# Performance work log

Hardware: AMD Instinct MI355X
Metric: run time of the kernel (lower is better)

## Reference

```python
import jax, jax.numpy as jnp
import numpy as np

H = W = 28
PI = np.pi


def _encoder(x, c1w, c1b, c2w, c2b):
    dn = ('NCHW', 'OIHW', 'NCHW')
    h = jax.lax.conv_general_dilated(x, c1w, (1, 1), 'SAME', dimension_numbers=dn)
    h = jax.nn.relu(h + c1b[None, :, None, None])
    h = jax.lax.conv_general_dilated(h, c2w, (2, 2), 'SAME', dimension_numbers=dn)
    return jax.nn.relu(h + c2b[None, :, None, None])


def _angles_deg(x):
    # Batched replacement of the per-image masked-point PCA loop:
    # masked 2x2 covariance + closed-form top eigenvector (same math as
    # torch.svd of the mean-centered selected points).
    B = x.shape[0]
    imgs = x.reshape(B, -1)                       # [B, 784]
    m = (imgs > 0.5).astype(x.dtype)              # boolean selection as weights
    xs = jnp.linspace(-14.0, 14.0, 28)
    ys = jnp.linspace(14.0, -14.0, 28)
    gx, gy = jnp.meshgrid(xs, ys)                 # 'xy' indexing, matches np.meshgrid
    gx = gx.reshape(-1)
    gy = gy.reshape(-1)                           # [784]
    n = jnp.maximum(m.sum(1), 1.0)                # [B]
    mx = (m * gx).sum(1) / n
    my = (m * gy).sum(1) / n
    dx = gx[None, :] - mx[:, None]                # [B, 784]
    dy = gy[None, :] - my[:, None]
    a = (m * dx * dx).sum(1)                      # unnormalized covariance entries
    b = (m * dx * dy).sum(1)
    c = (m * dy * dy).sum(1)
    lam = 0.5 * (a + c) + jnp.sqrt(0.25 * (a - c) ** 2 + b * b)  # top eigenvalue
    v1 = jnp.stack([b, lam - a], -1)              # two algebraic eigenvector forms
    v2 = jnp.stack([lam - c, b], -1)
    use1 = (v1 * v1).sum(-1) >= (v2 * v2).sum(-1)
    v = jnp.where(use1[:, None], v1, v2)
    v = jnp.where((v * v).sum(-1, keepdims=True) < 1e-12,
                  jnp.array([1.0, 0.0], dtype=x.dtype), v)  # isotropic fallback
    return jnp.arctan2(v[:, 1], v[:, 0]) * (180.0 / PI)


def _rotate(x, angles_deg):
    # kornia.geometry.rotate: rotate by angle degrees (CCW) about image center,
    # bilinear interpolation, zero padding. x: [B,1,H,W].
    B = x.shape[0]
    th = angles_deg * (PI / 180.0)
    cs = jnp.cos(th)[:, None, None]
    sn = jnp.sin(th)[:, None, None]
    yy, xx = jnp.meshgrid(jnp.arange(H, dtype=x.dtype),
                          jnp.arange(W, dtype=x.dtype), indexing='ij')
    cx = (W - 1) / 2.0
    cy = (H - 1) / 2.0
    dxp = xx - cx
    dyp = yy - cy
    # inverse warp (OpenCV getRotationMatrix2D convention)
    sx = cs * dxp + sn * dyp + cx                 # [B,H,W] source coords
    sy = -sn * dxp + cs * dyp + cy
    x0 = jnp.floor(sx)
    y0 = jnp.floor(sy)
    wx1 = sx - x0
    wx0 = 1.0 - wx1
    wy1 = sy - y0
    wy0 = 1.0 - wy1
    img = x.reshape(B, -1)                        # single channel

    def samp(yi, xi):
        valid = (xi >= 0) & (xi <= W - 1) & (yi >= 0) & (yi <= H - 1)
        xi_ = jnp.clip(xi, 0, W - 1).astype(jnp.int32)
        yi_ = jnp.clip(yi, 0, H - 1).astype(jnp.int32)
        idx = (yi_ * W + xi_).reshape(B, -1)
        vals = jnp.take_along_axis(img, idx, axis=1).reshape(B, H, W)
        return vals * valid.astype(x.dtype)

    out = (samp(y0, x0) * wy0 * wx0 + samp(y0, x0 + 1) * wy0 * wx1 +
           samp(y0 + 1, x0) * wy1 * wx0 + samp(y0 + 1, x0 + 1) * wy1 * wx1)
    return out[:, None, :, :]


def setup_inputs() -> dict:
    key = jax.random.key(0)
    ks = jax.random.split(key, 5)
    B = 2048
    x = jax.random.uniform(ks[0], (B, 1, 28, 28), jnp.float32)
    conv1_w = jax.random.normal(ks[1], (32, 1, 3, 3), jnp.float32) * 0.1
    conv1_b = jnp.zeros((32,), jnp.float32)
    conv2_w = jax.random.normal(ks[2], (64, 32, 3, 3), jnp.float32) * 0.05
    conv2_b = jnp.zeros((64,), jnp.float32)
    pred_w = jax.random.normal(ks[3], (64 * 14 * 14, 10), jnp.float32) * 0.01
    pred_b = jnp.zeros((10,), jnp.float32)
    return {'x': x, 'conv1_w': conv1_w, 'conv1_b': conv1_b,
            'conv2_w': conv2_w, 'conv2_b': conv2_b,
            'pred_w': pred_w, 'pred_b': pred_b}


def reference(x, conv1_w, conv1_b, conv2_w, conv2_b, pred_w, pred_b):
    angles = jax.lax.stop_gradient(_angles_deg(x))  # original detaches angles
    x_canonized = _rotate(x, -angles)
    reps = _encoder(x_canonized, conv1_w, conv1_b, conv2_w, conv2_b)
    reps = reps.reshape(x.shape[0], -1)             # [B, 12544]
    return reps @ pred_w + pred_b                   # [B, 10]
```

## Files before the change

### kernel.cpp

```cpp
#include <hip/hip_runtime.h>
#include <math.h>

typedef __attribute__((ext_vector_type(8))) short short8;
typedef __attribute__((ext_vector_type(4))) float f32x4;
typedef __attribute__((ext_vector_type(8))) _Float16 half8;
typedef __attribute__((ext_vector_type(4))) _Float16 half4;
typedef __attribute__((ext_vector_type(2))) _Float16 half2v;
typedef __attribute__((ext_vector_type(4))) unsigned int uint4v;

#define H1_OFF   3840
#define H1_ROWB  1920
#define LDS_BYTES (H1_OFF + 29*H1_ROWB)
#define RED_OFF  25344

__device__ __forceinline__ int h1_byte(int y, int x, int chunk) {
    int b = H1_OFF + y*H1_ROWB + x*64 + chunk*16;
    return b ^ (((x >> 1) & 7) << 4);
}

__device__ __forceinline__ half2v hmax2(half2v a) {
#if defined(__has_builtin) && __has_builtin(__builtin_elementwise_max)
    half2v z = {(_Float16)0.0f, (_Float16)0.0f};
    return __builtin_elementwise_max(a, z);
#else
    half2v r;
    r[0] = a[0] > (_Float16)0.0f ? a[0] : (_Float16)0.0f;
    r[1] = a[1] > (_Float16)0.0f ? a[1] : (_Float16)0.0f;
    return r;
#endif
}

__global__ __launch_bounds__(256) void prep_kernel(
    const float* __restrict__ w1, const float* __restrict__ b1,
    const float* __restrict__ w2, const float* __restrict__ pw,
    unsigned* __restrict__ w1pk,
    unsigned short* __restrict__ w2frag, unsigned short* __restrict__ pwt2)
{
    const int NW1 = 160;
    const int NW2 = 9*4*64*8;
    const int NPW = 10*12544;
    for (int idx = blockIdx.x*256 + threadIdx.x; idx < NW1 + NW2 + NPW; idx += gridDim.x*256) {
        if (idx < NW1) {
            half2v h;
            if (idx < 144) {
                int c2 = idx / 9, k = idx - 9*c2;
                h[0] = (_Float16)w1[(2*c2)*9 + k];
                h[1] = (_Float16)w1[(2*c2+1)*9 + k];
            } else {
                int c2 = idx - 144;
                h[0] = (_Float16)b1[2*c2];
                h[1] = (_Float16)b1[2*c2+1];
            }
            w1pk[idx] = __builtin_bit_cast(unsigned, h);
        } else if (idx < NW1 + NW2) {
            int d = idx - NW1;
            int m = d & 7;
            int l = (d >> 3) & 63;
            int f = d >> 9;
            int oct = f & 3;
            int kk = f >> 2;
            int oc = oct*16 + (l & 15);
            int c  = (l >> 4)*8 + m;
            _Float16 h = (_Float16)w2[(oc*32 + c)*9 + kk];
            w2frag[d] = __builtin_bit_cast(unsigned short, h);
        } else {
            int j = idx - NW1 - NW2;
            int k = j / 12544;
            int i2 = j - k*12544;
            _Float16 h = (_Float16)pw[i2*10 + k];
            pwt2[k*12544 + i2] = __builtin_bit_cast(unsigned short, h);
        }
    }
}

__global__ __launch_bounds__(256) void angle_kernel(
    const float* __restrict__ x, float2* __restrict__ csn)
{
    const int b = blockIdx.x;
    const int t = threadIdx.x;
    const float* xb = x + b * 784;

    double S = 0, Sx = 0, Sy = 0, Sxx = 0, Sxy = 0, Syy = 0;
    for (int p = t; p < 784; p += 256) {
        float v = xb[p];
        if (v > 0.5f) {
            int j = p / 28;
            int i = p - j * 28;
            double gx = -14.0 + i * (28.0 / 27.0);
            double gy =  14.0 - j * (28.0 / 27.0);
            S   += 1.0;
            Sx  += gx;   Sy  += gy;
            Sxx += gx * gx; Sxy += gx * gy; Syy += gy * gy;
        }
    }
    #pragma unroll
    for (int off = 32; off; off >>= 1) {
        S   += __shfl_down(S, off);
        Sx  += __shfl_down(Sx, off);
        Sy  += __shfl_down(Sy, off);
        Sxx += __shfl_down(Sxx, off);
        Sxy += __shfl_down(Sxy, off);
        Syy += __shfl_down(Syy, off);
    }
    __shared__ double red[4][6];
    const int lane = t & 63, w = t >> 6;
    if (lane == 0) {
        red[w][0] = S; red[w][1] = Sx; red[w][2] = Sy;
        red[w][3] = Sxx; red[w][4] = Sxy; red[w][5] = Syy;
    }
    __syncthreads();
    if (t == 0) {
        S   = red[0][0] + red[1][0] + red[2][0] + red[3][0];
        Sx  = red[0][1] + red[1][1] + red[2][1] + red[3][1];
        Sy  = red[0][2] + red[1][2] + red[2][2] + red[3][2];
        Sxx = red[0][3] + red[1][3] + red[2][3] + red[3][3];
        Sxy = red[0][4] + red[1][4] + red[2][4] + red[3][4];
        Syy = red[0][5] + red[1][5] + red[2][5] + red[3][5];

        double n  = (S < 1.0) ? 1.0 : S;
        double mx = Sx / n, my = Sy / n;
        double a  = Sxx - 2.0 * mx * Sx + mx * mx * S;
        double bb = Sxy - mx * Sy - my * Sx + mx * my * S;
        double cc = Syy - 2.0 * my * Sy + my * my * S;
        double lam = 0.5 * (a + cc) + sqrt(0.25 * (a - cc) * (a - cc) + bb * bb);
        double v1x = bb, v1y = lam - a;
        double v2x = lam - cc, v2y = bb;
        double n1 = v1x * v1x + v1y * v1y;
        double n2 = v2x * v2x + v2y * v2y;
        double vx, vy;
        if (n1 >= n2) { vx = v1x; vy = v1y; } else { vx = v2x; vy = v2y; }
        if (vx * vx + vy * vy < 1e-12) { vx = 1.0; vy = 0.0; }
        double th = -atan2(vy, vx);
        csn[b] = make_float2((float)cos(th), (float)sin(th));
    }
}

__global__ __launch_bounds__(1024, 8) void fused_kernel(
    const float* __restrict__ x,
    const unsigned* __restrict__ w1pk,
    const float* __restrict__ b2,
    const unsigned short* __restrict__ w2frag,
    const unsigned short* __restrict__ pwt2,
    const float* __restrict__ pb,
    const float2* __restrict__ csn,
    float* __restrict__ out)
{
    __shared__ __align__(16) char lds[LDS_BYTES];
    float* rotf = (float*)lds;
    float* imgf = (float*)(lds + H1_OFF);
    _Float16* reps16 = (_Float16*)lds;
    float* red  = (float*)(lds + RED_OFF);

    const int b = blockIdx.x;
    const int t = threadIdx.x;
    const int lane = t & 63;
    const int wv = t >> 6;
    const int l15 = lane & 15;
    const int g   = lane >> 4;

    const float* xb = x + b*784;
    int ty = t/28, tx = t - ty*28;
    if (t < 784) {
        imgf[ty*32 + tx] = xb[t];
    }
    if (t < 960) rotf[t] = 0.0f;
    __syncthreads();

    if (t < 784) {
        const float2 cn = csn[b];
        const float cs = cn.x, sn = cn.y;
        float dxp = (float)tx - 13.5f;
        float dyp = (float)ty - 13.5f;
        float sx =  cs*dxp + sn*dyp + 13.5f;
        float sy = -sn*dxp + cs*dyp + 13.5f;
        float x0 = floorf(sx), y0 = floorf(sy);
        float wx1 = sx - x0, wx0 = 1.0f - wx1;
        float wy1 = sy - y0, wy0 = 1.0f - wy1;
        int ix0 = (int)x0, iy0 = (int)y0;
        int ix1 = ix0 + 1, iy1 = iy0 + 1;
        int cx0 = min(max(ix0, 0), 27), cy0 = min(max(iy0, 0), 27);
        int cx1 = min(max(ix1, 0), 27), cy1 = min(max(iy1, 0), 27);
        bool vx0 = (ix0 >= 0) & (ix0 <= 27);
        bool vx1 = (ix1 >= 0) & (ix1 <= 27);
        bool vy0 = (iy0 >= 0) & (iy0 <= 27);
        bool vy1 = (iy1 >= 0) & (iy1 <= 27);
        float a00 = imgf[cy0*32 + cx0];
        float a01 = imgf[cy0*32 + cx1];
        float a10 = imgf[cy1*32 + cx0];
        float a11 = imgf[cy1*32 + cx1];
        float v00 = (vx0 & vy0) ? a00 : 0.f;
        float v01 = (vx1 & vy0) ? a01 : 0.f;
        float v10 = (vx0 & vy1) ? a10 : 0.f;
        float v11 = (vx1 & vy1) ? a11 : 0.f;
        float r = v00*wy0*wx0 + v01*wy0*wx1 + v10*wy1*wx0 + v11*wy1*wx1;
        rotf[(ty + 1)*32 + (tx + 1)] = r;
    }
    __syncthreads();

    if (t < 228) {
        short8 z8 = {0,0,0,0,0,0,0,0};
        int cell = t >> 2;
        int chunk = t & 3;
        int y, xx;
        if (cell < 29) { y = 28; xx = cell; } else { y = cell - 29; xx = 28; }
        *(short8*)(lds + h1_byte(y, xx, chunk)) = z8;
    }

    if (lane < 49) {
        int p = wv*49 + lane;
        int py = p/28, px = p - py*28;
        const float* rp = rotf + py*32 + px;
        half2v rs[9];
        {
            float rv[9] = { rp[0],  rp[1],  rp[2],
                            rp[32], rp[33], rp[34],
                            rp[64], rp[65], rp[66] };
            #pragma unroll
            for (int m = 0; m < 9; ++m) {
                _Float16 h = (_Float16)rv[m];
                rs[m][0] = h; rs[m][1] = h;
            }
        }
        half2v acc2[16];
        #pragma unroll
        for (int c2 = 0; c2 < 16; ++c2) {
            half2v a = __builtin_bit_cast(half2v, w1pk[144 + c2]);
            #pragma unroll
            for (int k = 0; k < 9; ++k) {
                half2v w = __builtin_bit_cast(half2v, w1pk[c2*9 + k]);
                a = w * rs[k] + a;
            }
            acc2[c2] = hmax2(a);
        }
        #pragma unroll
        for (int c8 = 0; c8 < 4; ++c8) {
            uint4v vh;
            #pragma unroll
            for (int j = 0; j < 4; ++j)
                vh[j] = __builtin_bit_cast(unsigned, acc2[c8*4 + j]);
            *(uint4v*)(lds + h1_byte(py, px, c8)) = vh;
        }
    }
    __syncthreads();

    const int oct = wv & 3;
    const int trow = wv >> 2;
    const int nq = (trow == 0) ? 4 : 3;
    int oyq[4], oxq[4];
    #pragma unroll
    for (int q = 0; q < 4; ++q) {
        int sp = (trow + 4*q)*16 + l15;
        sp = sp > 195 ? 195 : sp;
        oyq[q] = sp/14;
        oxq[q] = sp - 14*oyq[q];
    }
    f32x4 acc[4];
    #pragma unroll
    for (int q = 0; q < 4; ++q) acc[q] = (f32x4){0.f, 0.f, 0.f, 0.f};

    for (int kk = 0; kk < 9; ++kk) {
        int ky = kk/3;
        int kx = kk - ky*3;
        half8 bh = *(const half8*)(w2frag + (kk*4 + oct)*512 + lane*8);
        #pragma unroll
        for (int q = 0; q < 4; ++q) {
            if (q < nq) {
                int y = 2*oyq[q] + ky, xx = 2*oxq[q] + kx;
                half8 ah = *(const half8*)(lds + h1_byte(y, xx, g));
                acc[q] = __builtin_amdgcn_mfma_f32_16x16x32_f16(ah, bh, acc[q], 0, 0, 0);
            }
        }
    }
    __syncthreads();

    {
        int oc = oct*16 + l15;
        float bias = b2[oc];
        #pragma unroll
        for (int q = 0; q < 4; ++q) {
            if (q < nq) {
                int sp0 = (trow + 4*q)*16 + 4*g;
                if (sp0 + 3 < 196) {
                    half4 v;
                    #pragma unroll
                    for (int j = 0; j < 4; ++j)
                        v[j] = (_Float16)fmaxf(acc[q][j] + bias, 0.0f);
                    *(half4*)(reps16 + oc*196 + sp0) = v;
                }
            }
        }
    }
    __syncthreads();

    float a10[10];
    #pragma unroll
    for (int k = 0; k < 10; ++k) a10[k] = 0.0f;
    const unsigned* pw32 = (const unsigned*)pwt2;
    const unsigned* rp32 = (const unsigned*)reps16;
    for (int ip = t; ip < 6272; ip += 1024) {
        unsigned rv = rp32[ip];
#if defined(__has_builtin) && __has_builtin(__builtin_amdgcn_fdot2)
        half2v rh = __builtin_bit_cast(half2v, rv);
        #pragma unroll
        for (int k = 0; k < 10; ++k) {
            half2v ph = __builtin_bit_cast(half2v, pw32[k*6272 + ip]);
            a10[k] = __builtin_amdgcn_fdot2(rh, ph, a10[k], false);
        }
#else
        half2v rh = __builtin_bit_cast(half2v, rv);
        float r0 = (float)rh[0], r1 = (float)rh[1];
        #pragma unroll
        for (int k = 0; k < 10; ++k) {
            half2v ph = __builtin_bit_cast(half2v, pw32[k*6272 + ip]);
            a10[k] = fmaf(r0, (float)ph[0], fmaf(r1, (float)ph[1], a10[k]));
        }
#endif
    }
    #pragma unroll
    for (int k = 0; k < 10; ++k) {
        float v = a10[k];
        #pragma unroll
        for (int off = 32; off; off >>= 1) v += __shfl_down(v, off);
        a10[k] = v;
    }
    if (lane == 0) {
        #pragma unroll
        for (int k = 0; k < 10; ++k) red[wv*10 + k] = a10[k];
    }
    __syncthreads();
    if (t < 10) {
        float s = pb[t];
        #pragma unroll
        for (int w = 0; w < 16; ++w) s += red[w*10 + t];
        out[b*10 + t] = s;
    }
}

extern "C" void kernel_launch(void* const* d_in, const int* in_sizes, int n_in,
                              void* d_out, int out_size, void* d_ws, size_t ws_size,
                              hipStream_t stream)
{
    const float* x   = (const float*)d_in[0];
    const float* w1  = (const float*)d_in[1];
    const float* b1  = (const float*)d_in[2];
    const float* w2  = (const float*)d_in[3];
    const float* b2  = (const float*)d_in[4];
    const float* pw  = (const float*)d_in[5];
    const float* pb  = (const float*)d_in[6];
    float* out = (float*)d_out;

    const int B = in_sizes[0] / 784;

    char* wsb = (char*)d_ws;
    float2* csn = (float2*)wsb;
    unsigned* w1pk = (unsigned*)(wsb + (size_t)B*8);
    unsigned short* w2frag = (unsigned short*)(wsb + (size_t)B*8 + 640);
    unsigned short* pwt2   = (unsigned short*)(wsb + (size_t)B*8 + 640 + 36864);

    prep_kernel<<<563, 256, 0, stream>>>(w1, b1, w2, pw, w1pk, w2frag, pwt2);
    angle_kernel<<<B, 256, 0, stream>>>(x, csn);
    fused_kernel<<<B, 1024, 0, stream>>>(x, w1pk, b2, w2frag, pwt2, pb, csn, out);
}
```

Baseline: 81.79 us.

## Fuse angle PCA reduction into main kernel and drop separate angle launch

Moves the per-image masked covariance reduction and eigenvector computation into the fused kernel, using the already-loaded image pixels, wave shuffles and an LDS cross-wave reduce. This removes one kernel launch, the second read of x, and the csn round-trip through global memory. It also replaces atan2/cos/sin with direct normalisation of the eigenvector. The cost is an extra barrier and a serial double-precision tail inside the main kernel, with LDS slots reused for the reduction.

```diff
diff --git a/kernel.cpp b/kernel.cpp
--- a/kernel.cpp
+++ b/kernel.cpp
@@ -11,6 +11,8 @@
 #define H1_OFF   3840
 #define H1_ROWB  1920
 #define LDS_BYTES (H1_OFF + 29*H1_ROWB)
+#define ANG_OFF  7424
+#define CSN_OFF  8192
 #define RED_OFF  25344
 
 __device__ __forceinline__ int h1_byte(int y, int x, int chunk) {
@@ -73,68 +75,6 @@
     }
 }
 
-__global__ __launch_bounds__(256) void angle_kernel(
-    const float* __restrict__ x, float2* __restrict__ csn)
-{
-    const int b = blockIdx.x;
-    const int t = threadIdx.x;
-    const float* xb = x + b * 784;
-
-    double S = 0, Sx = 0, Sy = 0, Sxx = 0, Sxy = 0, Syy = 0;
-    for (int p = t; p < 784; p += 256) {
-        float v = xb[p];
-        if (v > 0.5f) {
-            int j = p / 28;
-            int i = p - j * 28;
-            double gx = -14.0 + i * (28.0 / 27.0);
-            double gy =  14.0 - j * (28.0 / 27.0);
-            S   += 1.0;
-            Sx  += gx;   Sy  += gy;
-            Sxx += gx * gx; Sxy += gx * gy; Syy += gy * gy;
-        }
-    }
-    #pragma unroll
-    for (int off = 32; off; off >>= 1) {
-        S   += __shfl_down(S, off);
-        Sx  += __shfl_down(Sx, off);
-        Sy  += __shfl_down(Sy, off);
-        Sxx += __shfl_down(Sxx, off);
-        Sxy += __shfl_down(Sxy, off);
-        Syy += __shfl_down(Syy, off);
-    }
-    __shared__ double red[4][6];
-    const int lane = t & 63, w = t >> 6;
-    if (lane == 0) {
-        red[w][0] = S; red[w][1] = Sx; red[w][2] = Sy;
-        red[w][3] = Sxx; red[w][4] = Sxy; red[w][5] = Syy;
-    }
-    __syncthreads();
-    if (t == 0) {
-        S   = red[0][0] + red[1][0] + red[2][0] + red[3][0];
-        Sx  = red[0][1] + red[1][1] + red[2][1] + red[3][1];
-        Sy  = red[0][2] + red[1][2] + red[2][2] + red[3][2];
-        Sxx = red[0][3] + red[1][3] + red[2][3] + red[3][3];
-        Sxy = red[0][4] + red[1][4] + red[2][4] + red[3][4];
-        Syy = red[0][5] + red[1][5] + red[2][5] + red[3][5];
-
-        double n  = (S < 1.0) ? 1.0 : S;
-        double mx = Sx / n, my = Sy / n;
-        double a  = Sxx - 2.0 * mx * Sx + mx * mx * S;
-        double bb = Sxy - mx * Sy - my * Sx + mx * my * S;
-        double cc = Syy - 2.0 * my * Sy + my * my * S;
-        double lam = 0.5 * (a + cc) + sqrt(0.25 * (a - cc) * (a - cc) + bb * bb);
-        double v1x = bb, v1y = lam - a;
-        double v2x = lam - cc, v2y = bb;
-        double n1 = v1x * v1x + v1y * v1y;
-        double n2 = v2x * v2x + v2y * v2y;
-        double vx, vy;
-        if (n1 >= n2) { vx = v1x; vy = v1y; } else { vx = v2x; vy = v2y; }
-        if (vx * vx + vy * vy < 1e-12) { vx = 1.0; vy = 0.0; }
-        double th = -atan2(vy, vx);
-        csn[b] = make_float2((float)cos(th), (float)sin(th));
-    }
-}
-
 __global__ __launch_bounds__(1024, 8) void fused_kernel(
     const float* __restrict__ x,
     const unsigned* __restrict__ w1pk,
@@ -142,12 +82,13 @@
     const unsigned short* __restrict__ w2frag,
     const unsigned short* __restrict__ pwt2,
     const float* __restrict__ pb,
-    const float2* __restrict__ csn,
     float* __restrict__ out)
 {
     __shared__ __align__(16) char lds[LDS_BYTES];
     float* rotf = (float*)lds;
     float* imgf = (float*)(lds + H1_OFF);
+    double* angS = (double*)(lds + ANG_OFF);
+    float2* csnL = (float2*)(lds + CSN_OFF);
     _Float16* reps16 = (_Float16*)lds;
     float* red  = (float*)(lds + RED_OFF);
 
@@ -159,15 +100,73 @@
     const int g   = lane >> 4;
 
     const float* xb = x + b*784;
+    float xv = 0.0f;
     int ty = t/28, tx = t - ty*28;
     if (t < 784) {
-        imgf[ty*32 + tx] = xb[t];
-    }
-    if (t < 960) rotf[t] = 0.0f;
+        xv = xb[t];
+        imgf[ty*32 + tx] = xv;
+    }
+    {
+        double S=0, Sx=0, Sy=0, Sxx=0, Sxy=0, Syy=0;
+        if (t < 784 && xv > 0.5f) {
+            double gx = -14.0 + tx * (28.0 / 27.0);
+            double gy =  14.0 - ty * (28.0 / 27.0);
+            S = 1.0; Sx = gx; Sy = gy;
+            Sxx = gx*gx; Sxy = gx*gy; Syy = gy*gy;
+        }
+        #pragma unroll
+        for (int off = 32; off; off >>= 1) {
+            S   += __shfl_down(S, off);
+            Sx  += __shfl_down(Sx, off);
+            Sy  += __shfl_down(Sy, off);
+            Sxx += __shfl_down(Sxx, off);
+            Sxy += __shfl_down(Sxy, off);
+            Syy += __shfl_down(Syy, off);
+        }
+        if (lane == 0) {
+            angS[wv*6+0] = S;  angS[wv*6+1] = Sx;  angS[wv*6+2] = Sy;
+            angS[wv*6+3] = Sxx; angS[wv*6+4] = Sxy; angS[wv*6+5] = Syy;
+        }
+    }
+    __syncthreads();
+
+    if (t >= 64) {
+        rotf[t - 64] = 0.0f;
+    } else if (t < 16) {
+        double S = angS[t*6+0], Sx = angS[t*6+1], Sy = angS[t*6+2];
+        double Sxx = angS[t*6+3], Sxy = angS[t*6+4], Syy = angS[t*6+5];
+        #pragma unroll
+        for (int off = 8; off; off >>= 1) {
+            S   += __shfl_down(S, off);
+            Sx  += __shfl_down(Sx, off);
+            Sy  += __shfl_down(Sy, off);
+            Sxx += __shfl_down(Sxx, off);
+            Sxy += __shfl_down(Sxy, off);
+            Syy += __shfl_down(Syy, off);
+        }
+        if (t == 0) {
+            double n  = (S < 1.0) ? 1.0 : S;
+            double mx = Sx / n, my = Sy / n;
+            double a  = Sxx - 2.0*mx*Sx + mx*mx*S;
+            double bb = Sxy - mx*Sy - my*Sx + mx*my*S;
+            double cc = Syy - 2.0*my*Sy + my*my*S;
+            double lam = 0.5*(a + cc) + sqrt(0.25*(a - cc)*(a - cc) + bb*bb);
+            double v1x = bb, v1y = lam - a;
+            double v2x = lam - cc, v2y = bb;
+            double n1 = v1x*v1x + v1y*v1y;
+            double n2 = v2x*v2x + v2y*v2y;
+            double vx, vy, nn;
+            if (n1 >= n2) { vx = v1x; vy = v1y; nn = n1; }
+            else          { vx = v2x; vy = v2y; nn = n2; }
+            if (nn < 1e-12) { vx = 1.0; vy = 0.0; nn = 1.0; }
+            double rinv = 1.0 / sqrt(nn);
+            csnL[0] = make_float2((float)(vx*rinv), (float)(-vy*rinv));
+        }
+    }
     __syncthreads();
 
     if (t < 784) {
-        const float2 cn = csn[b];
+        const float2 cn = csnL[0];
         const float cs = cn.x, sn = cn.y;
         float dxp = (float)tx - 13.5f;
         float dyp = (float)ty - 13.5f;
@@ -205,7 +204,6 @@
         if (cell < 29) { y = 28; xx = cell; } else { y = cell - 29; xx = 28; }
         *(short8*)(lds + h1_byte(y, xx, chunk)) = z8;
     }
-
     if (lane < 49) {
         int p = wv*49 + lane;
         int py = p/28, px = p - py*28;
@@ -352,12 +350,10 @@
     const int B = in_sizes[0] / 784;
 
     char* wsb = (char*)d_ws;
-    float2* csn = (float2*)wsb;
-    unsigned* w1pk = (unsigned*)(wsb + (size_t)B*8);
-    unsigned short* w2frag = (unsigned short*)(wsb + (size_t)B*8 + 640);
-    unsigned short* pwt2   = (unsigned short*)(wsb + (size_t)B*8 + 640 + 36864);
+    unsigned* w1pk = (unsigned*)wsb;
+    unsigned short* w2frag = (unsigned short*)(wsb + 640);
+    unsigned short* pwt2   = (unsigned short*)(wsb + 640 + 36864);
 
     prep_kernel<<<563, 256, 0, stream>>>(w1, b1, w2, pw, w1pk, w2frag, pwt2);
-    angle_kernel<<<B, 256, 0, stream>>>(x, csn);
-    fused_kernel<<<B, 1024, 0, stream>>>(x, w1pk, b2, w2frag, pwt2, pb, csn, out);
-}
+    fused_kernel<<<B, 1024, 0, stream>>>(x, w1pk, b2, w2frag, pwt2, pb, out);
+}
```

Result: slower. 94.84 us (+16.0%).
